# Kernel tuning notes

Hardware: AMD Instinct MI355X
Metric: run time of the kernel (lower is better)

Reference implementation:

```python
import jax, jax.numpy as jnp
import numpy as np

B, T, C, H = 4, 2048, 1024, 16
D = C // H  # head_dim = 64

def setup_inputs() -> dict:
    key = jax.random.key(0)
    ks = jax.random.split(key, 5)
    scale = 1.0 / np.sqrt(C)
    return {
        "x": jax.random.normal(ks[0], (B, T, C), dtype=jnp.float32),
        "Wq": jax.random.normal(ks[1], (C, C), dtype=jnp.float32) * scale,
        "Wk": jax.random.normal(ks[2], (C, C), dtype=jnp.float32) * scale,
        "Wv": jax.random.normal(ks[3], (C, C), dtype=jnp.float32) * scale,
        "Wo": jax.random.normal(ks[4], (C, C), dtype=jnp.float32) * scale,
        "bo": jnp.zeros((C,), dtype=jnp.float32),
    }

def reference(x, Wq, Wk, Wv, Wo, bo):
    Bx, Tx, Cx = x.shape
    # projections -> [B, H, T, D]
    def split_heads(y):
        return y.reshape(Bx, Tx, H, D).transpose(0, 2, 1, 3)
    Q = split_heads(x @ Wq)
    K = split_heads(x @ Wk)
    V = split_heads(x @ Wv)
    # scaled dot-product with causal mask: [B, H, T, T]
    scores = jnp.einsum('bhqd,bhkd->bhqk', Q, K) / jnp.sqrt(jnp.asarray(D, x.dtype))
    causal = jnp.tril(jnp.ones((Tx, Tx), dtype=bool))
    scores = jnp.where(causal, scores, -jnp.inf)
    weights = jax.nn.softmax(scores, axis=-1)
    attn = jnp.einsum('bhqk,bhkd->bhqd', weights, V)  # [B, H, T, D]
    out = attn.transpose(0, 2, 1, 3).reshape(Bx, Tx, Cx)
    return out @ Wo + bo
```

## Files before the change

### kernel.cpp

```cpp
#include <hip/hip_runtime.h>
#include <hip/hip_bf16.h>
#include <cmath>

typedef __bf16 bf16;
typedef __bf16 bf16x8 __attribute__((ext_vector_type(8)));
typedef __bf16 bf16x4v __attribute__((ext_vector_type(4)));
typedef float f32x4 __attribute__((ext_vector_type(4)));

#define B_ 4
#define T_ 2048
#define C_ 1024
#define H_ 16
#define D_ 64
#define BT_ 8192
#define LOG2E 1.4426950408889634f

__device__ __forceinline__ void async_cp16(const void* g, void* l) {
  __builtin_amdgcn_global_load_lds(
      (__attribute__((address_space(1))) void*)g,
      (__attribute__((address_space(3))) void*)l, 16, 0, 0);
}

__device__ __forceinline__ f32x4 mfma16(bf16x8 a, bf16x8 b, f32x4 c) {
  return __builtin_amdgcn_mfma_f32_16x16x32_bf16(a, b, c, 0, 0, 0);
}

__global__ __launch_bounds__(256) void cast_x_kernel(
    const float* __restrict__ in, bf16* __restrict__ out, int n4) {
  int i = blockIdx.x * 256 + threadIdx.x;
  if (i >= n4) return;
  float4 v = ((const float4*)in)[i];
  bf16x4v o = {(bf16)v.x, (bf16)v.y, (bf16)v.z, (bf16)v.w};
  ((bf16x4v*)out)[i] = o;
}

__global__ __launch_bounds__(256) void transpose_cast4_kernel(
    const float* __restrict__ Wq, const float* __restrict__ Wk,
    const float* __restrict__ Wv, const float* __restrict__ Wo,
    bf16* __restrict__ dst) {
  __shared__ float tile[32][33];
  const int z = blockIdx.z;
  const float* W = (z == 0) ? Wq : (z == 1) ? Wk : (z == 2) ? Wv : Wo;
  bf16* Wt = dst + (size_t)z * 1048576;
  const int x = threadIdx.x, y = threadIdx.y;
  const int n0 = blockIdx.x * 32, k0 = blockIdx.y * 32;
#pragma unroll
  for (int j = 0; j < 32; j += 8)
    tile[y + j][x] = W[(size_t)(k0 + y + j) * C_ + n0 + x];
  __syncthreads();
#pragma unroll
  for (int j = 0; j < 32; j += 8)
    Wt[(size_t)(n0 + y + j) * C_ + k0 + x] = (bf16)tile[x][y + j];
}

template <int F32OUT>
__global__ __launch_bounds__(256, 3) void gemm_bt_kernel(
    const bf16* __restrict__ A, const bf16* __restrict__ Bt,
    void* __restrict__ Cv, const float* __restrict__ bias,
    int M, int N, int K) {
  __shared__ __align__(16) bf16 As[128 * 64];
  __shared__ __align__(16) bf16 Bs[128 * 64];
  const int t = threadIdx.x;
  const int lane = t & 63;
  const int wave = t >> 6;
  const int quad = lane >> 4;
  const int l15 = lane & 15;
  const int l7 = l15 & 7;
  const int m0 = blockIdx.y * 128;
  const int n0 = blockIdx.x * 128;
  const int wm = (wave >> 1) * 64;
  const int wn = (wave & 1) * 64;

  const int sr8 = lane >> 3;
  const int sc = (lane & 7) ^ sr8;
  const bf16* Ag = A + (size_t)(m0 + wave * 32 + sr8) * K + sc * 8;
  const bf16* Bg = Bt + (size_t)(n0 + wave * 32 + sr8) * K + sc * 8;
  bf16* Ad = As + wave * 2048 + lane * 8;
  bf16* Bd = Bs + wave * 2048 + lane * 8;

  f32x4 acc[4][4] = {};

  for (int kt = 0; kt < K; kt += 64) {
#pragma unroll
    for (int i = 0; i < 4; i++) {
      async_cp16(Ag + kt + (size_t)(i * 8) * K, Ad + i * 512);
      async_cp16(Bg + kt + (size_t)(i * 8) * K, Bd + i * 512);
    }
    __syncthreads();
#pragma unroll
    for (int ks = 0; ks < 2; ks++) {
      bf16x8 af[4], bfr[4];
#pragma unroll
      for (int i = 0; i < 4; i++)
        af[i] = *(const bf16x8*)&As[(wm + i * 16 + l15) * 64 +
                                    (((ks * 4 + quad) ^ l7) * 8)];
#pragma unroll
      for (int j = 0; j < 4; j++)
        bfr[j] = *(const bf16x8*)&Bs[(wn + j * 16 + l15) * 64 +
                                     (((ks * 4 + quad) ^ l7) * 8)];
#pragma unroll
      for (int i = 0; i < 4; i++)
#pragma unroll
        for (int j = 0; j < 4; j++)
          acc[i][j] = mfma16(af[i], bfr[j], acc[i][j]);
    }
    __syncthreads();
  }

#pragma unroll
  for (int i = 0; i < 4; i++) {
    const int gr = m0 + wm + i * 16 + quad * 4;
#pragma unroll
    for (int j = 0; j < 4; j++) {
      const int gc = n0 + wn + j * 16 + l15;
      const float bv = F32OUT ? bias[gc] : 0.0f;
#pragma unroll
      for (int r = 0; r < 4; r++) {
        const float v = acc[i][j][r] + bv;
        if (F32OUT)
          ((float*)Cv)[(size_t)(gr + r) * N + gc] = v;
        else
          ((bf16*)Cv)[(size_t)(gr + r) * N + gc] = (bf16)v;
      }
    }
  }
}

__global__ __launch_bounds__(256, 3) void flash_attn_kernel(
    const bf16* __restrict__ qk, const bf16* __restrict__ vt,
    bf16* __restrict__ attn) {
  __shared__ __align__(16) char smem[51200];
  bf16* KsB = (bf16*)smem;
  bf16* VsB = (bf16*)(smem + 16384);
  bf16* Ps = (bf16*)(smem + 32768);

  const int t = threadIdx.x;
  const int lane = t & 63;
  const int wave = t >> 6;
  const int quad = lane >> 4;
  const int l15 = lane & 15;
  const int l7 = l15 & 7;
  const int bx = blockIdx.x;
  const int qt = 15 - (bx >> 6);
  const int bh = bx & 63;
  const int b = bh >> 4;
  const int h = bh & 15;

  const bf16* Qg = qk + (size_t)b * T_ * 2048 + h * 64;
  const bf16* Kg = qk + (size_t)b * T_ * 2048 + 1024 + h * 64;
  const bf16* Vg = vt + (size_t)h * 64 * BT_ + b * T_;

  bf16x8 qf[2][2];
  const int qrow0 = qt * 128 + wave * 32;
#pragma unroll
  for (int mt = 0; mt < 2; mt++)
#pragma unroll
    for (int ks = 0; ks < 2; ks++) {
      bf16x8 v = *(const bf16x8*)(Qg + (size_t)(qrow0 + mt * 16 + l15) * 2048 +
                                  ks * 32 + quad * 8);
#pragma unroll
      for (int j = 0; j < 8; j++) v[j] = (bf16)((float)v[j] * 0.125f);
      qf[mt][ks] = v;
    }

  f32x4 o_acc[4][2] = {};
  f32x4 l4[2] = {};

  const int sr8 = lane >> 3;
  const int sc = (lane & 7) ^ sr8;

  auto stage = [&](int j64, int buf) {
    const int k0 = j64 * 64;
    bf16* KL = KsB + buf * 4096 + wave * 1024 + lane * 8;
    const bf16* KG = Kg + (size_t)(k0 + wave * 16 + sr8) * 2048 + sc * 8;
    async_cp16(KG, KL);
    async_cp16(KG + (size_t)8 * 2048, KL + 512);
    bf16* VL = VsB + buf * 4096 + wave * 1024 + lane * 8;
    const bf16* VG = Vg + (size_t)(wave * 16 + sr8) * BT_ + k0 + sc * 8;
    async_cp16(VG, VL);
    async_cp16(VG + (size_t)8 * BT_, VL + 512);
  };

  const int S = 2 * qt + 2;
  stage(0, 0);

  for (int s = 0; s < S; s++) {
    __syncthreads();
    if (s + 1 < S) stage(s + 1, (s + 1) & 1);
    const bf16* Kb = KsB + (s & 1) * 4096;
    const bf16* Vb = VsB + (s & 1) * 4096;
    const int k0 = s * 64;
    const bool diag = (s >= 2 * qt);

    bf16x4v p[2][4];
#pragma unroll
    for (int kt = 0; kt < 4; kt++) {
      const bf16x8 kf0 =
          *(const bf16x8*)&Kb[(kt * 16 + l15) * 64 + ((quad ^ l7) * 8)];
      const bf16x8 kf1 =
          *(const bf16x8*)&Kb[(kt * 16 + l15) * 64 + (((4 + quad) ^ l7) * 8)];
#pragma unroll
      for (int mt = 0; mt < 2; mt++) {
        f32x4 sv = mfma16(kf0, qf[mt][0], f32x4{0.f, 0.f, 0.f, 0.f});
        sv = mfma16(kf1, qf[mt][1], sv);
        if (diag) {
          const int qg = qt * 128 + wave * 32 + mt * 16 + l15;
#pragma unroll
          for (int i = 0; i < 4; i++)
            if (k0 + kt * 16 + quad * 4 + i > qg) sv[i] = -INFINITY;
        }
        f32x4 e;
#pragma unroll
        for (int i = 0; i < 4; i++)
          e[i] = __builtin_amdgcn_exp2f(sv[i] * LOG2E);
        l4[mt] += e;
        p[mt][kt] = bf16x4v{(bf16)e[0], (bf16)e[1], (bf16)e[2], (bf16)e[3]};
      }
    }

#pragma unroll
    for (int mt = 0; mt < 2; mt++) {
      const int row = wave * 32 + mt * 16 + l15;
#pragma unroll
      for (int kt = 0; kt < 4; kt++)
        *(bf16x4v*)&Ps[row * 72 + kt * 16 + quad * 4] = p[mt][kt];
    }

#pragma unroll
    for (int ks2 = 0; ks2 < 2; ks2++) {
      bf16x8 pa[2], vb[4];
#pragma unroll
      for (int mt = 0; mt < 2; mt++)
        pa[mt] = *(const bf16x8*)&Ps[(wave * 32 + mt * 16 + l15) * 72 +
                                     ks2 * 32 + quad * 8];
#pragma unroll
      for (int dt = 0; dt < 4; dt++)
        vb[dt] = *(const bf16x8*)&Vb[(dt * 16 + l15) * 64 +
                                     (((ks2 * 4 + quad) ^ l7) * 8)];
#pragma unroll
      for (int dt = 0; dt < 4; dt++)
#pragma unroll
        for (int mt = 0; mt < 2; mt++)
          o_acc[dt][mt] = mfma16(vb[dt], pa[mt], o_acc[dt][mt]);
    }
  }

  float inv[2];
#pragma unroll
  for (int mt = 0; mt < 2; mt++) {
    float l = l4[mt][0] + l4[mt][1] + l4[mt][2] + l4[mt][3];
    l += __shfl_xor(l, 16, 64);
    l += __shfl_xor(l, 32, 64);
    inv[mt] = 1.0f / l;
  }
#pragma unroll
  for (int dt = 0; dt < 4; dt++)
#pragma unroll
    for (int mt = 0; mt < 2; mt++) {
      const int q = qt * 128 + wave * 32 + mt * 16 + l15;
      bf16x4v o = {(bf16)(o_acc[dt][mt][0] * inv[mt]),
                   (bf16)(o_acc[dt][mt][1] * inv[mt]),
                   (bf16)(o_acc[dt][mt][2] * inv[mt]),
                   (bf16)(o_acc[dt][mt][3] * inv[mt])};
      *(bf16x4v*)(attn + (size_t)(b * T_ + q) * 1024 + h * 64 + dt * 16 +
                  quad * 4) = o;
    }
}

extern "C" void kernel_launch(void* const* d_in, const int* in_sizes, int n_in,
                              void* d_out, int out_size, void* d_ws,
                              size_t ws_size, hipStream_t stream) {
  const float* x = (const float*)d_in[0];
  const float* Wq = (const float*)d_in[1];
  const float* Wk = (const float*)d_in[2];
  const float* Wv = (const float*)d_in[3];
  const float* Wo = (const float*)d_in[4];
  const float* bo = (const float*)d_in[5];
  float* out = (float*)d_out;

  char* ws = (char*)d_ws;
  bf16* xb = (bf16*)(ws);
  bf16* qkb = (bf16*)(ws + 16777216);
  bf16* vtb = (bf16*)(ws + 50331648);
  bf16* attn = (bf16*)(ws + 67108864);
  bf16* wqkvT = (bf16*)(ws + 83886080);
  bf16* woT = (bf16*)(ws + 90177536);

  cast_x_kernel<<<8192, 256, 0, stream>>>(x, xb, 2097152);

  transpose_cast4_kernel<<<dim3(32, 32, 4), dim3(32, 8), 0, stream>>>(
      Wq, Wk, Wv, Wo, wqkvT);

  gemm_bt_kernel<0><<<dim3(16, 64), 256, 0, stream>>>(
      xb, wqkvT, (void*)qkb, nullptr, 8192, 2048, 1024);

  gemm_bt_kernel<0><<<dim3(64, 8), 256, 0, stream>>>(
      wqkvT + 2 * 1024 * 1024, xb, (void*)vtb, nullptr, 1024, 8192, 1024);

  flash_attn_kernel<<<1024, 256, 0, stream>>>(qkb, vtb, attn);

  gemm_bt_kernel<1><<<dim3(8, 64), 256, 0, stream>>>(
      attn, woT, (void*)out, bo, 8192, 1024, 1024);
}
```

Baseline: 239.8 us.

## Double-buffer GEMM tiles, merge prep and QKV launches, fold log2e into Q scale

The GEMM is turned into a device function with double-buffered LDS tiles. It prefetches the next K tile before computing the current one, which removes one barrier per iteration. The cast and transpose kernels become one prep launch, and the Q/K and V^T GEMMs share a single launch of 1536 blocks, which cuts launch gaps and tail effects. The softmax scale now folds log2e into the Q prescale, saving one multiply per exp. The cost is that LDS use doubles and occupancy drops from 3 to 2 blocks per CU.

```diff
diff --git a/kernel.cpp b/kernel.cpp
--- a/kernel.cpp
+++ b/kernel.cpp
@@ -25,49 +25,48 @@
   return __builtin_amdgcn_mfma_f32_16x16x32_bf16(a, b, c, 0, 0, 0);
 }
 
-__global__ __launch_bounds__(256) void cast_x_kernel(
-    const float* __restrict__ in, bf16* __restrict__ out, int n4) {
-  int i = blockIdx.x * 256 + threadIdx.x;
-  if (i >= n4) return;
-  float4 v = ((const float4*)in)[i];
-  bf16x4v o = {(bf16)v.x, (bf16)v.y, (bf16)v.z, (bf16)v.w};
-  ((bf16x4v*)out)[i] = o;
-}
-
-__global__ __launch_bounds__(256) void transpose_cast4_kernel(
-    const float* __restrict__ Wq, const float* __restrict__ Wk,
-    const float* __restrict__ Wv, const float* __restrict__ Wo,
-    bf16* __restrict__ dst) {
+__global__ __launch_bounds__(256) void prep_kernel(
+    const float* __restrict__ x, const float* __restrict__ Wq,
+    const float* __restrict__ Wk, const float* __restrict__ Wv,
+    const float* __restrict__ Wo, bf16* __restrict__ xb,
+    bf16* __restrict__ wt) {
   __shared__ float tile[32][33];
-  const int z = blockIdx.z;
+  const int id = blockIdx.x;
+  const int t = threadIdx.x;
+  if (id < 8192) {
+    const int i = id * 256 + t;
+    float4 v = ((const float4*)x)[i];
+    bf16x4v o = {(bf16)v.x, (bf16)v.y, (bf16)v.z, (bf16)v.w};
+    ((bf16x4v*)xb)[i] = o;
+    return;
+  }
+  const int id2 = id - 8192;
+  const int z = id2 >> 10;
   const float* W = (z == 0) ? Wq : (z == 1) ? Wk : (z == 2) ? Wv : Wo;
-  bf16* Wt = dst + (size_t)z * 1048576;
-  const int x = threadIdx.x, y = threadIdx.y;
-  const int n0 = blockIdx.x * 32, k0 = blockIdx.y * 32;
+  bf16* Wt = wt + (size_t)z * 1048576;
+  const int bx = id2 & 31, by = (id2 >> 5) & 31;
+  const int xx = t & 31, yy = t >> 5;
+  const int n0 = bx * 32, k0 = by * 32;
 #pragma unroll
   for (int j = 0; j < 32; j += 8)
-    tile[y + j][x] = W[(size_t)(k0 + y + j) * C_ + n0 + x];
+    tile[yy + j][xx] = W[(size_t)(k0 + yy + j) * C_ + n0 + xx];
   __syncthreads();
 #pragma unroll
   for (int j = 0; j < 32; j += 8)
-    Wt[(size_t)(n0 + y + j) * C_ + k0 + x] = (bf16)tile[x][y + j];
+    Wt[(size_t)(n0 + yy + j) * C_ + k0 + xx] = (bf16)tile[xx][yy + j];
 }
 
 template <int F32OUT>
-__global__ __launch_bounds__(256, 3) void gemm_bt_kernel(
+__device__ __forceinline__ void gemm_tile_db(
     const bf16* __restrict__ A, const bf16* __restrict__ Bt,
-    void* __restrict__ Cv, const float* __restrict__ bias,
-    int M, int N, int K) {
-  __shared__ __align__(16) bf16 As[128 * 64];
-  __shared__ __align__(16) bf16 Bs[128 * 64];
+    void* __restrict__ Cv, const float* __restrict__ bias, int M, int N, int K,
+    int m0, int n0, bf16* As, bf16* Bs) {
   const int t = threadIdx.x;
   const int lane = t & 63;
   const int wave = t >> 6;
   const int quad = lane >> 4;
   const int l15 = lane & 15;
   const int l7 = l15 & 7;
-  const int m0 = blockIdx.y * 128;
-  const int n0 = blockIdx.x * 128;
   const int wm = (wave >> 1) * 64;
   const int wn = (wave & 1) * 64;
 
@@ -75,28 +74,36 @@
   const int sc = (lane & 7) ^ sr8;
   const bf16* Ag = A + (size_t)(m0 + wave * 32 + sr8) * K + sc * 8;
   const bf16* Bg = Bt + (size_t)(n0 + wave * 32 + sr8) * K + sc * 8;
-  bf16* Ad = As + wave * 2048 + lane * 8;
-  bf16* Bd = Bs + wave * 2048 + lane * 8;
+
+  const int niter = K >> 6;
+  auto stage = [&](int kt, int buf) {
+    bf16* Ad = As + buf * 8192 + wave * 2048 + lane * 8;
+    bf16* Bd = Bs + buf * 8192 + wave * 2048 + lane * 8;
+#pragma unroll
+    for (int i = 0; i < 4; i++) {
+      async_cp16(Ag + kt * 64 + (size_t)(i * 8) * K, Ad + i * 512);
+      async_cp16(Bg + kt * 64 + (size_t)(i * 8) * K, Bd + i * 512);
+    }
+  };
 
   f32x4 acc[4][4] = {};
-
-  for (int kt = 0; kt < K; kt += 64) {
-#pragma unroll
-    for (int i = 0; i < 4; i++) {
-      async_cp16(Ag + kt + (size_t)(i * 8) * K, Ad + i * 512);
-      async_cp16(Bg + kt + (size_t)(i * 8) * K, Bd + i * 512);
-    }
+  stage(0, 0);
+
+  for (int kt = 0; kt < niter; kt++) {
     __syncthreads();
+    if (kt + 1 < niter) stage(kt + 1, (kt + 1) & 1);
+    const bf16* Ab = As + (kt & 1) * 8192;
+    const bf16* Bb = Bs + (kt & 1) * 8192;
 #pragma unroll
     for (int ks = 0; ks < 2; ks++) {
       bf16x8 af[4], bfr[4];
 #pragma unroll
       for (int i = 0; i < 4; i++)
-        af[i] = *(const bf16x8*)&As[(wm + i * 16 + l15) * 64 +
+        af[i] = *(const bf16x8*)&Ab[(wm + i * 16 + l15) * 64 +
                                     (((ks * 4 + quad) ^ l7) * 8)];
 #pragma unroll
       for (int j = 0; j < 4; j++)
-        bfr[j] = *(const bf16x8*)&Bs[(wn + j * 16 + l15) * 64 +
+        bfr[j] = *(const bf16x8*)&Bb[(wn + j * 16 + l15) * 64 +
                                      (((ks * 4 + quad) ^ l7) * 8)];
 #pragma unroll
       for (int i = 0; i < 4; i++)
@@ -104,7 +111,6 @@
         for (int j = 0; j < 4; j++)
           acc[i][j] = mfma16(af[i], bfr[j], acc[i][j]);
     }
-    __syncthreads();
   }
 
 #pragma unroll
@@ -124,6 +130,32 @@
       }
     }
   }
+}
+
+__global__ __launch_bounds__(256, 2) void qkv_gemm_kernel(
+    const bf16* __restrict__ xb, const bf16* __restrict__ wqkvT,
+    bf16* __restrict__ qkb, bf16* __restrict__ vtb) {
+  __shared__ __align__(16) bf16 As[2 * 8192];
+  __shared__ __align__(16) bf16 Bs[2 * 8192];
+  int id = blockIdx.x;
+  if (id < 1024) {
+    gemm_tile_db<0>(xb, wqkvT, (void*)qkb, nullptr, 8192, 2048, 1024,
+                    (id >> 4) * 128, (id & 15) * 128, As, Bs);
+  } else {
+    id -= 1024;
+    gemm_tile_db<0>(wqkvT + 2 * 1024 * 1024, xb, (void*)vtb, nullptr, 1024,
+                    8192, 1024, (id >> 6) * 128, (id & 63) * 128, As, Bs);
+  }
+}
+
+__global__ __launch_bounds__(256, 2) void out_gemm_kernel(
+    const bf16* __restrict__ attn, const bf16* __restrict__ woT,
+    float* __restrict__ out, const float* __restrict__ bo) {
+  __shared__ __align__(16) bf16 As[2 * 8192];
+  __shared__ __align__(16) bf16 Bs[2 * 8192];
+  const int id = blockIdx.x;
+  gemm_tile_db<1>(attn, woT, (void*)out, bo, 8192, 1024, 1024,
+                  (id >> 3) * 128, (id & 7) * 128, As, Bs);
 }
 
 __global__ __launch_bounds__(256, 3) void flash_attn_kernel(
@@ -150,6 +182,7 @@
   const bf16* Kg = qk + (size_t)b * T_ * 2048 + 1024 + h * 64;
   const bf16* Vg = vt + (size_t)h * 64 * BT_ + b * T_;
 
+  const float QSCALE = 0.125f * LOG2E;
   bf16x8 qf[2][2];
   const int qrow0 = qt * 128 + wave * 32;
 #pragma unroll
@@ -159,7 +192,7 @@
       bf16x8 v = *(const bf16x8*)(Qg + (size_t)(qrow0 + mt * 16 + l15) * 2048 +
                                   ks * 32 + quad * 8);
 #pragma unroll
-      for (int j = 0; j < 8; j++) v[j] = (bf16)((float)v[j] * 0.125f);
+      for (int j = 0; j < 8; j++) v[j] = (bf16)((float)v[j] * QSCALE);
       qf[mt][ks] = v;
     }
 
@@ -211,8 +244,7 @@
         }
         f32x4 e;
 #pragma unroll
-        for (int i = 0; i < 4; i++)
-          e[i] = __builtin_amdgcn_exp2f(sv[i] * LOG2E);
+        for (int i = 0; i < 4; i++) e[i] = __builtin_amdgcn_exp2f(sv[i]);
         l4[mt] += e;
         p[mt][kt] = bf16x4v{(bf16)e[0], (bf16)e[1], (bf16)e[2], (bf16)e[3]};
       }
@@ -284,21 +316,13 @@
   bf16* vtb = (bf16*)(ws + 50331648);
   bf16* attn = (bf16*)(ws + 67108864);
   bf16* wqkvT = (bf16*)(ws + 83886080);
-  bf16* woT = (bf16*)(ws + 90177536);
-
-  cast_x_kernel<<<8192, 256, 0, stream>>>(x, xb, 2097152);
-
-  transpose_cast4_kernel<<<dim3(32, 32, 4), dim3(32, 8), 0, stream>>>(
-      Wq, Wk, Wv, Wo, wqkvT);
-
-  gemm_bt_kernel<0><<<dim3(16, 64), 256, 0, stream>>>(
-      xb, wqkvT, (void*)qkb, nullptr, 8192, 2048, 1024);
-
-  gemm_bt_kernel<0><<<dim3(64, 8), 256, 0, stream>>>(
-      wqkvT + 2 * 1024 * 1024, xb, (void*)vtb, nullptr, 1024, 8192, 1024);
+
+  prep_kernel<<<12288, 256, 0, stream>>>(x, Wq, Wk, Wv, Wo, xb, wqkvT);
+
+  qkv_gemm_kernel<<<1536, 256, 0, stream>>>(xb, wqkvT, qkb, vtb);
 
   flash_attn_kernel<<<1024, 256, 0, stream>>>(qkb, vtb, attn);
 
-  gemm_bt_kernel<1><<<dim3(8, 64), 256, 0, stream>>>(
-      attn, woT, (void*)out, bo, 8192, 1024, 1024);
-}
+  out_gemm_kernel<<<512, 256, 0, stream>>>(attn, wqkvT + 3 * 1024 * 1024, out,
+                                           bo);
+}
```

Measured after the change: 234.0 us. -2.4%, faster.
